# Optimization experiments

Measured on AMD Instinct MI355X. Metric: run time of the kernel, lower is better.

The kernel has to match this reference:

```python
import jax, jax.numpy as jnp
import numpy as np

B, S, H = 8, 2048, 768      # batch, seq_len, hidden_size
N = 512                     # spans per example
MAXW = 30                   # max span width (length in [0, MAXW-1] -> width <= MAXW)


def setup_inputs() -> dict:
    key = jax.random.key(0)
    k1, k2, k3, k4 = jax.random.split(key, 4)
    embeddings = jax.random.normal(k1, (B, S, H), dtype=jnp.float32)
    starts = jax.random.randint(k2, (B, N), 0, S - MAXW)          # span starts
    lengths = jax.random.randint(k3, (B, N), 0, MAXW)             # end = start + length
    w = jax.random.normal(k4, (H, 1), dtype=jnp.float32) * 0.02   # nn.Linear(hidden, 1) weight (transposed)
    b = jnp.zeros((1,), dtype=jnp.float32)                        # linear bias
    return {"embeddings": embeddings, "w": w, "b": b, "starts": starts, "lengths": lengths}


def reference(embeddings, w, b, starts, lengths):
    # Vectorized ragged span pooling: gather up to MAXW tokens per span,
    # masked softmax over attention scores, then concat [start, end, attn].
    ends = starts + lengths                                  # inclusive end index
    offs = jnp.arange(MAXW)                                  # (W,)
    positions = starts[..., None] + offs                     # (B, N, W)
    mask = offs[None, None, :] <= lengths[..., None]         # (B, N, W) valid-token mask

    gather = jax.vmap(lambda e, p: e[p])                     # per-example gather
    span_emb = gather(embeddings, positions)                 # (B, N, W, H)

    scores = span_emb @ w + b                                # (B, N, W, 1)
    scores = jnp.where(mask[..., None], scores, -jnp.inf)
    attn_w = jax.nn.softmax(scores, axis=2)                  # masked softmax over span width
    attn_out = jnp.sum(attn_w * span_emb, axis=2)            # (B, N, H)

    start_emb = gather(embeddings, starts)                   # (B, N, H)
    end_emb = gather(embeddings, ends)                       # (B, N, H)
    return jnp.concatenate([start_emb, end_emb, attn_out], axis=-1)  # (B, N, 3H)
```

## Files before the change

kernel.cpp:

```cpp
#include <hip/hip_runtime.h>
#include <hip/hip_bf16.h>
#include <math.h>

#define BB 8
#define SS 2048
#define HH 768
#define NN 512
#define MAXW 30

#define GEMV_BLOCKS (BB * SS / 4)

__global__ __launch_bounds__(256) void prep_kernel(
    const float* __restrict__ emb,
    const float* __restrict__ w,
    const float* __restrict__ bias,
    const int*   __restrict__ starts,
    float*       __restrict__ scores,
    int*         __restrict__ order,
    int gemv_blocks)
{
    const int tid = threadIdx.x;
    if ((int)blockIdx.x < gemv_blocks) {
        const int wv = tid >> 6, lane = tid & 63;
        const int token = blockIdx.x * 4 + wv;
        const float* row = emb + (size_t)token * HH;
        const int h0 = lane * 4;
        float acc = 0.f;
        #pragma unroll
        for (int k = 0; k < 3; ++k) {
            float4 e4 = *reinterpret_cast<const float4*>(row + h0 + k * 256);
            float4 w4 = *reinterpret_cast<const float4*>(w + h0 + k * 256);
            acc += e4.x * w4.x + e4.y * w4.y + e4.z * w4.z + e4.w * w4.w;
        }
        #pragma unroll
        for (int off = 32; off; off >>= 1) acc += __shfl_xor(acc, off);
        if (lane == 0) scores[token] = acc + bias[0];
    } else {
        const int b = blockIdx.x - gemv_blocks;
        __shared__ int hist[SS];
        __shared__ int partial[256];
        for (int i = tid; i < SS; i += 256) hist[i] = 0;
        __syncthreads();
        const int* st = starts + b * NN;
        for (int n = tid; n < NN; n += 256) atomicAdd(&hist[st[n]], 1);
        __syncthreads();
        const int base = tid * 8;
        int s = 0;
        #pragma unroll
        for (int k = 0; k < 8; ++k) s += hist[base + k];
        partial[tid] = s;
        __syncthreads();
        if (tid == 0) {
            int a = 0;
            for (int i = 0; i < 256; ++i) { int v = partial[i]; partial[i] = a; a += v; }
        }
        __syncthreads();
        int a = partial[tid];
        #pragma unroll
        for (int k = 0; k < 8; ++k) { int v = hist[base + k]; hist[base + k] = a; a += v; }
        __syncthreads();
        for (int n = tid; n < NN; n += 256) {
            int pos = atomicAdd(&hist[st[n]], 1);
            order[b * NN + pos] = n;
        }
    }
}

__global__ __launch_bounds__(256) void span_kernel(
    const float* __restrict__ emb,
    const float* __restrict__ w,
    const float* __restrict__ bias,
    const int*   __restrict__ starts,
    const int*   __restrict__ lengths,
    const int*   __restrict__ order,
    const float* __restrict__ scores,
    float*       __restrict__ out)
{
    const int tid  = threadIdx.x;
    const int wv   = tid >> 6;
    const int lane = tid & 63;
    const int bi   = blockIdx.x & 7;
    const int rank = ((int)blockIdx.x >> 3) * 4 + wv;
    const int n    = order ? order[bi * NN + rank] : rank;
    const int span = bi * NN + n;

    const int start = starts[span];
    const int len   = lengths[span];

    const float* ebase = emb + (size_t)bi * SS * HH + (size_t)start * HH;
    const int h0 = lane * 4;

    float sc;
    if (scores) {
        sc = (lane <= len) ? scores[bi * SS + start + lane] : -INFINITY;
    } else {
        float4 w0 = *reinterpret_cast<const float4*>(w + h0);
        float4 w1 = *reinterpret_cast<const float4*>(w + h0 + 256);
        float4 w2 = *reinterpret_cast<const float4*>(w + h0 + 512);
        sc = -INFINITY;
        for (int t = 0; t <= len; ++t) {
            const float* row = ebase + (size_t)t * HH;
            float4 v0 = *reinterpret_cast<const float4*>(row + h0);
            float4 v1 = *reinterpret_cast<const float4*>(row + h0 + 256);
            float4 v2 = *reinterpret_cast<const float4*>(row + h0 + 512);
            float d = v0.x * w0.x + v0.y * w0.y + v0.z * w0.z + v0.w * w0.w
                    + v1.x * w1.x + v1.y * w1.y + v1.z * w1.z + v1.w * w1.w
                    + v2.x * w2.x + v2.y * w2.y + v2.z * w2.z + v2.w * w2.w;
            #pragma unroll
            for (int off = 32; off; off >>= 1) d += __shfl_xor(d, off);
            if (lane == t) sc = d + bias[0];
        }
    }

    float m = sc;
    #pragma unroll
    for (int off = 32; off; off >>= 1) m = fmaxf(m, __shfl_xor(m, off));
    float e = (lane <= len) ? __expf(sc - m) : 0.f;
    float sum = e;
    #pragma unroll
    for (int off = 32; off; off >>= 1) sum += __shfl_xor(sum, off);
    const float p = e / sum;

    float* orow = out + (size_t)span * (3 * HH);
    float4 a0 = make_float4(0.f, 0.f, 0.f, 0.f);
    float4 a1 = a0, a2 = a0;
    const float* row = ebase;
    for (int t = 0; t <= len; ++t) {
        const float pt = __shfl(p, t);
        float4 v0 = *reinterpret_cast<const float4*>(row + h0);
        float4 v1 = *reinterpret_cast<const float4*>(row + h0 + 256);
        float4 v2 = *reinterpret_cast<const float4*>(row + h0 + 512);
        if (t == 0) {
            *reinterpret_cast<float4*>(orow + h0)       = v0;
            *reinterpret_cast<float4*>(orow + h0 + 256) = v1;
            *reinterpret_cast<float4*>(orow + h0 + 512) = v2;
        }
        if (t == len) {
            *reinterpret_cast<float4*>(orow + HH + h0)       = v0;
            *reinterpret_cast<float4*>(orow + HH + h0 + 256) = v1;
            *reinterpret_cast<float4*>(orow + HH + h0 + 512) = v2;
        }
        a0.x += pt * v0.x; a0.y += pt * v0.y; a0.z += pt * v0.z; a0.w += pt * v0.w;
        a1.x += pt * v1.x; a1.y += pt * v1.y; a1.z += pt * v1.z; a1.w += pt * v1.w;
        a2.x += pt * v2.x; a2.y += pt * v2.y; a2.z += pt * v2.z; a2.w += pt * v2.w;
        row += HH;
    }
    *reinterpret_cast<float4*>(orow + 2 * HH + h0)       = a0;
    *reinterpret_cast<float4*>(orow + 2 * HH + h0 + 256) = a1;
    *reinterpret_cast<float4*>(orow + 2 * HH + h0 + 512) = a2;
}

extern "C" void kernel_launch(void* const* d_in, const int* in_sizes, int n_in,
                              void* d_out, int out_size, void* d_ws, size_t ws_size,
                              hipStream_t stream) {
    const float* emb     = (const float*)d_in[0];
    const float* w       = (const float*)d_in[1];
    const float* bias    = (const float*)d_in[2];
    const int*   starts  = (const int*)d_in[3];
    const int*   lengths = (const int*)d_in[4];
    float*       out     = (float*)d_out;

    const size_t scores_bytes = (size_t)BB * SS * sizeof(float);
    const size_t order_bytes  = (size_t)BB * NN * sizeof(int);

    float* scores = nullptr;
    int*   order  = nullptr;
    if (ws_size >= scores_bytes + order_bytes) {
        scores = (float*)d_ws;
        order  = (int*)((char*)d_ws + scores_bytes);
    } else if (ws_size >= order_bytes) {
        order = (int*)d_ws;
    }

    if (scores || order) {
        const int gemv_blocks = scores ? GEMV_BLOCKS : 0;
        prep_kernel<<<dim3(gemv_blocks + BB), dim3(256), 0, stream>>>(
            emb, w, bias, starts, scores, order, gemv_blocks);
    }

    span_kernel<<<dim3(BB * NN / 4), dim3(256), 0, stream>>>(
        emb, w, bias, starts, lengths, order, scores, out);
}
```

Baseline: 37.60 us.

## Fuse span scoring into single-pass online-softmax pooling, drop global GEMV prepass

Removes the separate full-sequence GEMV that scored every token (reading all 50MB of embeddings) and instead computes scores on the fly inside the span kernel. An online softmax with running max and rescaling lets one pass over each span's rows produce both the scores and the weighted sum, with next-row prefetch. The sort prepass now uses a warp-shuffle scan instead of a serial scan. The trade-off is more ALU work and shuffle reductions per row, plus recomputed dot products for tokens shared by overlapping spans.

```diff
diff --git a/kernel.cpp b/kernel.cpp
--- a/kernel.cpp
+++ b/kernel.cpp
@@ -8,72 +8,58 @@
 #define NN 512
 #define MAXW 30
 
-#define GEMV_BLOCKS (BB * SS / 4)
+__global__ __launch_bounds__(256) void sort_spans_kernel(
+    const int* __restrict__ starts,
+    int*       __restrict__ order)
+{
+    const int b   = blockIdx.x;
+    const int tid = threadIdx.x;
+    __shared__ int hist[SS];
+    __shared__ int wsum[4];
 
-__global__ __launch_bounds__(256) void prep_kernel(
-    const float* __restrict__ emb,
-    const float* __restrict__ w,
-    const float* __restrict__ bias,
-    const int*   __restrict__ starts,
-    float*       __restrict__ scores,
-    int*         __restrict__ order,
-    int gemv_blocks)
-{
-    const int tid = threadIdx.x;
-    if ((int)blockIdx.x < gemv_blocks) {
-        const int wv = tid >> 6, lane = tid & 63;
-        const int token = blockIdx.x * 4 + wv;
-        const float* row = emb + (size_t)token * HH;
-        const int h0 = lane * 4;
-        float acc = 0.f;
-        #pragma unroll
-        for (int k = 0; k < 3; ++k) {
-            float4 e4 = *reinterpret_cast<const float4*>(row + h0 + k * 256);
-            float4 w4 = *reinterpret_cast<const float4*>(w + h0 + k * 256);
-            acc += e4.x * w4.x + e4.y * w4.y + e4.z * w4.z + e4.w * w4.w;
-        }
-        #pragma unroll
-        for (int off = 32; off; off >>= 1) acc += __shfl_xor(acc, off);
-        if (lane == 0) scores[token] = acc + bias[0];
-    } else {
-        const int b = blockIdx.x - gemv_blocks;
-        __shared__ int hist[SS];
-        __shared__ int partial[256];
-        for (int i = tid; i < SS; i += 256) hist[i] = 0;
-        __syncthreads();
-        const int* st = starts + b * NN;
-        for (int n = tid; n < NN; n += 256) atomicAdd(&hist[st[n]], 1);
-        __syncthreads();
-        const int base = tid * 8;
-        int s = 0;
-        #pragma unroll
-        for (int k = 0; k < 8; ++k) s += hist[base + k];
-        partial[tid] = s;
-        __syncthreads();
-        if (tid == 0) {
-            int a = 0;
-            for (int i = 0; i < 256; ++i) { int v = partial[i]; partial[i] = a; a += v; }
-        }
-        __syncthreads();
-        int a = partial[tid];
-        #pragma unroll
-        for (int k = 0; k < 8; ++k) { int v = hist[base + k]; hist[base + k] = a; a += v; }
-        __syncthreads();
-        for (int n = tid; n < NN; n += 256) {
-            int pos = atomicAdd(&hist[st[n]], 1);
-            order[b * NN + pos] = n;
-        }
+    for (int i = tid; i < SS; i += 256) hist[i] = 0;
+    __syncthreads();
+
+    const int* st = starts + b * NN;
+    for (int n = tid; n < NN; n += 256) atomicAdd(&hist[st[n]], 1);
+    __syncthreads();
+
+    const int base = tid * 8;
+    int cnt[8]; int s = 0;
+    #pragma unroll
+    for (int k = 0; k < 8; ++k) { cnt[k] = hist[base + k]; s += cnt[k]; }
+
+    const int lane = tid & 63, wv = tid >> 6;
+    int v = s;
+    #pragma unroll
+    for (int off = 1; off < 64; off <<= 1) {
+        int u = __shfl_up(v, off);
+        if (lane >= off) v += u;
+    }
+    if (lane == 63) wsum[wv] = v;
+    __syncthreads();
+    int wbase = 0;
+    #pragma unroll
+    for (int k = 0; k < 4; ++k) wbase += (k < wv) ? wsum[k] : 0;
+
+    int excl = wbase + v - s;
+    #pragma unroll
+    for (int k = 0; k < 8; ++k) { int c = cnt[k]; hist[base + k] = excl; excl += c; }
+    __syncthreads();
+
+    for (int n = tid; n < NN; n += 256) {
+        int pos = atomicAdd(&hist[st[n]], 1);
+        order[b * NN + pos] = n;
     }
 }
 
-__global__ __launch_bounds__(256) void span_kernel(
+__global__ __launch_bounds__(256) void span_fused_kernel(
     const float* __restrict__ emb,
     const float* __restrict__ w,
     const float* __restrict__ bias,
     const int*   __restrict__ starts,
     const int*   __restrict__ lengths,
     const int*   __restrict__ order,
-    const float* __restrict__ scores,
     float*       __restrict__ out)
 {
     const int tid  = threadIdx.x;
@@ -89,47 +75,51 @@
 
     const float* ebase = emb + (size_t)bi * SS * HH + (size_t)start * HH;
     const int h0 = lane * 4;
+    float* orow = out + (size_t)span * (3 * HH);
 
-    float sc;
-    if (scores) {
-        sc = (lane <= len) ? scores[bi * SS + start + lane] : -INFINITY;
-    } else {
-        float4 w0 = *reinterpret_cast<const float4*>(w + h0);
-        float4 w1 = *reinterpret_cast<const float4*>(w + h0 + 256);
-        float4 w2 = *reinterpret_cast<const float4*>(w + h0 + 512);
-        sc = -INFINITY;
-        for (int t = 0; t <= len; ++t) {
-            const float* row = ebase + (size_t)t * HH;
-            float4 v0 = *reinterpret_cast<const float4*>(row + h0);
-            float4 v1 = *reinterpret_cast<const float4*>(row + h0 + 256);
-            float4 v2 = *reinterpret_cast<const float4*>(row + h0 + 512);
-            float d = v0.x * w0.x + v0.y * w0.y + v0.z * w0.z + v0.w * w0.w
-                    + v1.x * w1.x + v1.y * w1.y + v1.z * w1.z + v1.w * w1.w
-                    + v2.x * w2.x + v2.y * w2.y + v2.z * w2.z + v2.w * w2.w;
-            #pragma unroll
-            for (int off = 32; off; off >>= 1) d += __shfl_xor(d, off);
-            if (lane == t) sc = d + bias[0];
+    const float4 w0 = *reinterpret_cast<const float4*>(w + h0);
+    const float4 w1 = *reinterpret_cast<const float4*>(w + h0 + 256);
+    const float4 w2 = *reinterpret_cast<const float4*>(w + h0 + 512);
+    const float bb = bias[0];
+
+    float m = -INFINITY, ssum = 0.f;
+    float4 a0 = make_float4(0.f, 0.f, 0.f, 0.f), a1 = a0, a2 = a0;
+
+    const float* row = ebase;
+    float4 v0 = *reinterpret_cast<const float4*>(row + h0);
+    float4 v1 = *reinterpret_cast<const float4*>(row + h0 + 256);
+    float4 v2 = *reinterpret_cast<const float4*>(row + h0 + 512);
+
+    for (int t = 0; t <= len; ++t) {
+        float4 n0, n1, n2;
+        if (t < len) {
+            const float* nr = row + HH;
+            n0 = *reinterpret_cast<const float4*>(nr + h0);
+            n1 = *reinterpret_cast<const float4*>(nr + h0 + 256);
+            n2 = *reinterpret_cast<const float4*>(nr + h0 + 512);
         }
-    }
 
-    float m = sc;
-    #pragma unroll
-    for (int off = 32; off; off >>= 1) m = fmaxf(m, __shfl_xor(m, off));
-    float e = (lane <= len) ? __expf(sc - m) : 0.f;
-    float sum = e;
-    #pragma unroll
-    for (int off = 32; off; off >>= 1) sum += __shfl_xor(sum, off);
-    const float p = e / sum;
+        float d = v0.x * w0.x + v0.y * w0.y + v0.z * w0.z + v0.w * w0.w
+                + v1.x * w1.x + v1.y * w1.y + v1.z * w1.z + v1.w * w1.w
+                + v2.x * w2.x + v2.y * w2.y + v2.z * w2.z + v2.w * w2.w;
+        #pragma unroll
+        for (int off = 32; off; off >>= 1) d += __shfl_xor(d, off);
+        d += bb;
 
-    float* orow = out + (size_t)span * (3 * HH);
-    float4 a0 = make_float4(0.f, 0.f, 0.f, 0.f);
-    float4 a1 = a0, a2 = a0;
-    const float* row = ebase;
-    for (int t = 0; t <= len; ++t) {
-        const float pt = __shfl(p, t);
-        float4 v0 = *reinterpret_cast<const float4*>(row + h0);
-        float4 v1 = *reinterpret_cast<const float4*>(row + h0 + 256);
-        float4 v2 = *reinterpret_cast<const float4*>(row + h0 + 512);
+        if (d > m) {
+            const float c = __expf(m - d);
+            ssum *= c;
+            a0.x *= c; a0.y *= c; a0.z *= c; a0.w *= c;
+            a1.x *= c; a1.y *= c; a1.z *= c; a1.w *= c;
+            a2.x *= c; a2.y *= c; a2.z *= c; a2.w *= c;
+            m = d;
+        }
+        const float pt = __expf(d - m);
+        ssum += pt;
+        a0.x += pt * v0.x; a0.y += pt * v0.y; a0.z += pt * v0.z; a0.w += pt * v0.w;
+        a1.x += pt * v1.x; a1.y += pt * v1.y; a1.z += pt * v1.z; a1.w += pt * v1.w;
+        a2.x += pt * v2.x; a2.y += pt * v2.y; a2.z += pt * v2.z; a2.w += pt * v2.w;
+
         if (t == 0) {
             *reinterpret_cast<float4*>(orow + h0)       = v0;
             *reinterpret_cast<float4*>(orow + h0 + 256) = v1;
@@ -140,11 +130,15 @@
             *reinterpret_cast<float4*>(orow + HH + h0 + 256) = v1;
             *reinterpret_cast<float4*>(orow + HH + h0 + 512) = v2;
         }
-        a0.x += pt * v0.x; a0.y += pt * v0.y; a0.z += pt * v0.z; a0.w += pt * v0.w;
-        a1.x += pt * v1.x; a1.y += pt * v1.y; a1.z += pt * v1.z; a1.w += pt * v1.w;
-        a2.x += pt * v2.x; a2.y += pt * v2.y; a2.z += pt * v2.z; a2.w += pt * v2.w;
+
+        v0 = n0; v1 = n1; v2 = n2;
         row += HH;
     }
+
+    const float inv = 1.f / ssum;
+    a0.x *= inv; a0.y *= inv; a0.z *= inv; a0.w *= inv;
+    a1.x *= inv; a1.y *= inv; a1.z *= inv; a1.w *= inv;
+    a2.x *= inv; a2.y *= inv; a2.z *= inv; a2.w *= inv;
     *reinterpret_cast<float4*>(orow + 2 * HH + h0)       = a0;
     *reinterpret_cast<float4*>(orow + 2 * HH + h0 + 256) = a1;
     *reinterpret_cast<float4*>(orow + 2 * HH + h0 + 512) = a2;
@@ -160,24 +154,12 @@
     const int*   lengths = (const int*)d_in[4];
     float*       out     = (float*)d_out;
 
-    const size_t scores_bytes = (size_t)BB * SS * sizeof(float);
-    const size_t order_bytes  = (size_t)BB * NN * sizeof(int);
-
-    float* scores = nullptr;
-    int*   order  = nullptr;
-    if (ws_size >= scores_bytes + order_bytes) {
-        scores = (float*)d_ws;
-        order  = (int*)((char*)d_ws + scores_bytes);
-    } else if (ws_size >= order_bytes) {
+    int* order = nullptr;
+    if (ws_size >= (size_t)(BB * NN * sizeof(int))) {
         order = (int*)d_ws;
+        sort_spans_kernel<<<dim3(BB), dim3(256), 0, stream>>>(starts, order);
     }
 
-    if (scores || order) {
-        const int gemv_blocks = scores ? GEMV_BLOCKS : 0;
-        prep_kernel<<<dim3(gemv_blocks + BB), dim3(256), 0, stream>>>(
-            emb, w, bias, starts, scores, order, gemv_blocks);
-    }
-
-    span_kernel<<<dim3(BB * NN / 4), dim3(256), 0, stream>>>(
-        emb, w, bias, starts, lengths, order, scores, out);
+    span_fused_kernel<<<dim3(BB * NN / 4), dim3(256), 0, stream>>>(
+        emb, w, bias, starts, lengths, order, out);
 }
```

Result: faster. 31.79 us (-15.5%).
